# Performance work log

Measured on AMD Instinct MI355X. Metric: run time of the kernel, lower is better.

Reference implementation:

```python
import jax, jax.numpy as jnp
import numpy as np

MARGIN = 0.0  # init kwarg margin=0


def setup_inputs() -> dict:
    key = jax.random.key(0)
    k1, k2 = jax.random.split(key)
    inputs = jax.random.normal(k1, (4096, 2048), dtype=jnp.float32)
    targets = jax.random.randint(k2, (4096,), 0, 64, dtype=jnp.int64)
    return {"inputs": inputs, "targets": targets}


def _last_true_index(cond):
    # cond: (n, n) bool. Original torch loop zeros leading True entries until one
    # remains -> keeps the LAST True index per row.
    n = cond.shape[1]
    return (n - 1) - jnp.argmax(cond[:, ::-1], axis=1)


def reference(inputs, targets):
    n = inputs.shape[0]
    INF = jnp.asarray(jnp.inf, dtype=inputs.dtype)

    # pairwise euclidean distances: ||xi||^2 + ||xj||^2 - 2 xi.xj, clamp, sqrt
    sq = jnp.sum(inputs * inputs, axis=1)
    dist = sq[:, None] + sq[None, :] - 2.0 * (inputs @ inputs.T)
    dist = jnp.sqrt(jnp.clip(dist, 1e-12))  # (n, n)

    same = targets[:, None] == targets[None, :]  # (n, n) same-label mask

    # hardest positive / hardest negative per row
    dist_ap = jnp.where(same, dist, -INF).max(axis=1)
    dist_an = jnp.where(same, INF, dist).min(axis=1)

    # tie-broken indices (last occurrence, matching the torch loop)
    p = _last_true_index((dist == dist_ap[:, None]) & same)      # hardest pos idx
    q = _last_true_index((dist == dist_an[:, None]) & (~same))   # hardest neg idx

    # an2 = dist(hardest_pos_i, hardest_neg_i)
    dist_an2 = dist[p, q]

    # maskc: labels differing from both anchor's label and hardest-negative's label
    lbl_q = targets[q]
    maskc = (targets[None, :] != targets[:, None]) & (targets[None, :] != lbl_q[:, None])

    dist_q = dist[q]  # (n, n): distance rows of the hardest negatives
    ok_min = jnp.where(maskc, dist_q, INF).min(axis=1)
    r = _last_true_index((dist_q == ok_min[:, None]) & maskc)

    dist_an3 = dist[jnp.arange(n), r]  # dist(anchor, third-class sample)
    dist_an4 = dist_q[jnp.arange(n), r]  # dist(hardest neg, third-class sample) == ok_min

    # MarginRankingLoss(margin, reduce=False) with y=1: relu(ap - an + margin)
    loss = jax.nn.relu(dist_ap - dist_an + MARGIN)
    loss3 = jnp.abs(dist_an - dist_an2)
    loss4 = jnp.abs(dist_an3 - dist_an4)
    return (loss + loss3 + loss4).sum() / n
```

## Files before the change

kernel.cpp:

```cpp
#include <hip/hip_runtime.h>
#include <hip/hip_bf16.h>
#include <cstdint>

#define N_DIM 4096
#define K_DIM 2048
#define NKT 32
#define QSCALE 24.0f
#define QINV (1.0f / 24.0f)

typedef float floatx4 __attribute__((ext_vector_type(4)));
typedef int intx4 __attribute__((ext_vector_type(4)));
typedef unsigned short ushort8 __attribute__((ext_vector_type(8)));
typedef unsigned long long ull;

__device__ __forceinline__ unsigned short f2bf(float f) {
    unsigned int u = __builtin_bit_cast(unsigned int, f);
    unsigned int r = (u + 0x7fffu + ((u >> 16) & 1u)) >> 16;
    return (unsigned short)r;
}

__device__ __forceinline__ float bf2f(unsigned short b) {
    return __uint_as_float(((unsigned)b) << 16);
}

__device__ __forceinline__ void gld_lds16(const void* g, void* l) {
    __builtin_amdgcn_global_load_lds(
        (const __attribute__((address_space(1))) unsigned int*)g,
        (__attribute__((address_space(3))) unsigned int*)l,
        16, 0, 0);
}

__global__ __launch_bounds__(256)
void prep_kernel(const float* __restrict__ X, const int* __restrict__ tgt,
                 char* __restrict__ Qt, int* __restrict__ sqi,
                 char* __restrict__ tgt8) {
    const int row = blockIdx.x;
    const int tid = threadIdx.x;
    if (row < 16) tgt8[row * 256 + tid] = (char)tgt[row * 256 + tid];
    const float* xr = X + (size_t)row * K_DIM;
    floatx4 a = *(const floatx4*)(xr + tid * 8);
    floatx4 b = *(const floatx4*)(xr + tid * 8 + 4);
    int s = 0;
    unsigned lo = 0, hi = 0;
#pragma unroll
    for (int e = 0; e < 4; ++e) {
        int v = __float2int_rn(a[e] * QSCALE);
        v = min(127, max(-127, v));
        s += v * v;
        lo |= ((unsigned)(v & 0xff)) << (8 * e);
        int w = __float2int_rn(b[e] * QSCALE);
        w = min(127, max(-127, w));
        s += w * w;
        hi |= ((unsigned)(w & 0xff)) << (8 * e);
    }
    *(int2*)(Qt + ((size_t)(tid >> 1) * 4096 + row) * 16 + (tid & 1) * 8) =
        make_int2((int)lo, (int)hi);
#pragma unroll
    for (int off = 32; off; off >>= 1) s += __shfl_down(s, off);
    __shared__ int wsum[4];
    const int wave = tid >> 6, lane = tid & 63;
    if (lane == 0) wsum[wave] = s;
    __syncthreads();
    if (tid == 0) sqi[row] = wsum[0] + wsum[1] + wsum[2] + wsum[3];
}

#define BAR() __builtin_amdgcn_s_barrier()
#define PRIO1() __builtin_amdgcn_s_setprio(1)
#define PRIO0() __builtin_amdgcn_s_setprio(0)
#define VMCNT4() asm volatile("s_waitcnt vmcnt(4)" ::: "memory")
#define VMCNT0() asm volatile("s_waitcnt vmcnt(0)" ::: "memory")
#define MM8(MHI, AF) { _Pragma("unroll") for (int n_ = 0; n_ < 4; ++n_) { \
    _Pragma("unroll") for (int m_ = 0; m_ < 4; ++m_) { \
        acc[MHI][n_][m_] = __builtin_amdgcn_mfma_i32_16x16x64_i8( \
            AF[m_], bfv[n_], acc[MHI][n_][m_], 0, 0, 0); } } }
#define KTB 262144
#define STG_ALL(KT, BB) { \
    gld_lds16(bSt + (size_t)(KT) * KTB,        lds + (BB) + 16384 + widB); \
    gld_lds16(bSt + (size_t)(KT) * KTB + 2048, lds + (BB) + 24576 + widB); \
    gld_lds16(aSt + (size_t)(KT) * KTB,        lds + (BB) + widB); \
    gld_lds16(aSt + (size_t)(KT) * KTB + 2048, lds + (BB) + 8192 + widB); }

__global__ __launch_bounds__(512, 2)
void gemm_dist(const char* __restrict__ Qt, const int* __restrict__ sqi,
               unsigned short* __restrict__ Db) {
    __shared__ char lds[131072];
    const int tid = threadIdx.x;
    const int wid = tid >> 6, lane = tid & 63;
    const int wr = wid >> 2, wc = wid & 3;
    const int fr = lane & 15, ksub = lane >> 4;
    const int widB = wid * 1024;

    int rA[4], rB[4];
#pragma unroll
    for (int m = 0; m < 4; ++m) rA[m] = (ksub * 128 + m * 16 + fr) * 16;
#pragma unroll
    for (int n = 0; n < 4; ++n) rB[n] = (ksub * 128 + (wc & 1) * 64 + n * 16 + fr) * 16;
    const int aRegOff = wr * 8192;
    const int bRegOff = 16384 + (wc >> 1) * 8192;

    const int swz = (blockIdx.x & 7) * 32 + (blockIdx.x >> 3);
    const int bi = swz >> 4, bj = swz & 15;
    const int rowC0 = bi * 256, colC0 = bj * 256;

    const int srow = tid & 127;
    const int sks = tid >> 7;
    const char* aSt = Qt + ((size_t)sks * 4096 + rowC0 + srow) * 16;
    const char* bSt = Qt + ((size_t)sks * 4096 + colC0 + srow) * 16;

    intx4 acc[2][4][4];
#pragma unroll
    for (int a0 = 0; a0 < 2; ++a0)
#pragma unroll
    for (int a1 = 0; a1 < 4; ++a1)
#pragma unroll
    for (int a2 = 0; a2 < 4; ++a2) acc[a0][a1][a2] = (intx4){0, 0, 0, 0};
    intx4 aflo[4], afhi[4], bfv[4];

    STG_ALL(0, 0);
    STG_ALL(1, 32768);
    VMCNT4();
    BAR();

    int cb = 0, sb = 65536;
    for (int t = 0; t < NKT; ++t) {
        const char* bufA = lds + cb + aRegOff;
        const char* bufBp = lds + cb + bRegOff;
#pragma unroll
        for (int m = 0; m < 4; ++m) aflo[m] = *(const intx4*)(bufA + rA[m]);
#pragma unroll
        for (int m = 0; m < 4; ++m) afhi[m] = *(const intx4*)(bufA + 1024 + rA[m]);
#pragma unroll
        for (int n = 0; n < 4; ++n) bfv[n] = *(const intx4*)(bufBp + rB[n]);
        if (t < NKT - 2) { STG_ALL(t + 2, sb); VMCNT4(); }
        else if (t == NKT - 2) { VMCNT0(); }
        BAR();
        PRIO1(); MM8(0, aflo); MM8(1, afhi); PRIO0();
        cb += 32768; if (cb >= 131072) cb = 0;
        sb += 32768; if (sb >= 131072) sb = 0;
    }

#pragma unroll
    for (int MH = 0; MH < 2; ++MH)
#pragma unroll
    for (int n = 0; n < 4; ++n) {
        const int col = colC0 + wc * 64 + n * 16 + fr;
        const int sqc = sqi[col];
#pragma unroll
        for (int m = 0; m < 4; ++m) {
            const int row0 = rowC0 + wr * 128 + MH * 64 + m * 16 + ksub * 4;
#pragma unroll
            for (int r = 0; r < 4; ++r) {
                const int v = sqi[row0 + r] + sqc - 2 * acc[MH][n][m][r];
                const float d = (v > 0) ? sqrtf((float)v) * QINV : 1e-6f;
                Db[(size_t)(row0 + r) * N_DIM + col] = f2bf(d);
            }
        }
    }
}

__global__ __launch_bounds__(256)
void stats_loss(const unsigned short* __restrict__ Db, const char* __restrict__ tgt8,
                float* __restrict__ lossArr) {
    const int i = blockIdx.x, tid = threadIdx.x;
    const int lane = tid & 63, wave = tid >> 6;
    const int ti = tgt8[i];
    const unsigned short* row = Db + (size_t)i * N_DIM;
    ull kmax = 0ULL, kmin = ~0ULL;
#pragma unroll
    for (int it = 0; it < 2; ++it) {
        const int j0 = (it * 256 + tid) * 8;
        ushort8 d = *(const ushort8*)(row + j0);
        const ull tl8 = *(const ull*)(tgt8 + j0);
#pragma unroll
        for (int e = 0; e < 8; ++e) {
            const int j = j0 + e;
            const int tl = (int)((tl8 >> (8 * e)) & 0xff);
            const ull db = (ull)d[e] << 32;
            if (tl == ti) { ull k = db | (unsigned)j;  if (k > kmax) kmax = k; }
            else          { ull k = db | (unsigned)~j; if (k < kmin) kmin = k; }
        }
    }
#pragma unroll
    for (int off = 32; off; off >>= 1) {
        ull o = __shfl_xor(kmax, off); if (o > kmax) kmax = o;
        o = __shfl_xor(kmin, off);     if (o < kmin) kmin = o;
    }
    __shared__ ull sW[8];
    if (lane == 0) { sW[wave] = kmax; sW[4 + wave] = kmin; }
    __syncthreads();
    ull km = sW[0], kn = sW[4];
#pragma unroll
    for (int w2 = 1; w2 < 4; ++w2) {
        if (sW[w2] > km) km = sW[w2];
        if (sW[4 + w2] < kn) kn = sW[4 + w2];
    }
    const float ap = bf2f((unsigned short)(km >> 32));
    const int p = (int)(unsigned)(km & 0xFFFFFFFFu);
    const float an = bf2f((unsigned short)(kn >> 32));
    const int q = (int)~(unsigned)(kn & 0xFFFFFFFFu);

    const int lq = tgt8[q];
    const unsigned short* rowq = Db + (size_t)q * N_DIM;
    ull kr = ~0ULL;
#pragma unroll
    for (int it = 0; it < 2; ++it) {
        const int j0 = (it * 256 + tid) * 8;
        ushort8 d = *(const ushort8*)(rowq + j0);
        const ull tl8 = *(const ull*)(tgt8 + j0);
#pragma unroll
        for (int e = 0; e < 8; ++e) {
            const int j = j0 + e;
            const int tl = (int)((tl8 >> (8 * e)) & 0xff);
            if (tl != ti && tl != lq) {
                ull k = ((ull)d[e] << 32) | (unsigned)~j;
                if (k < kr) kr = k;
            }
        }
    }
#pragma unroll
    for (int off = 32; off; off >>= 1) {
        ull o = __shfl_xor(kr, off); if (o < kr) kr = o;
    }
    __shared__ ull sR[4];
    if (lane == 0) sR[wave] = kr;
    __syncthreads();
    if (tid == 0) {
        ull kk = sR[0];
#pragma unroll
        for (int w2 = 1; w2 < 4; ++w2) if (sR[w2] < kk) kk = sR[w2];
        const float okmin = bf2f((unsigned short)(kk >> 32));
        const int r = (int)~(unsigned)(kk & 0xFFFFFFFFu);
        const float an2 = bf2f(Db[(size_t)p * N_DIM + q]);
        const float an3 = bf2f(Db[(size_t)i * N_DIM + r]);
        lossArr[i] = fmaxf(ap - an, 0.f) + fabsf(an - an2) + fabsf(an3 - okmin);
    }
}

__global__ __launch_bounds__(256)
void finred(const float* __restrict__ lossArr, float* __restrict__ out) {
    const int tid = threadIdx.x;
    float s = 0.f;
    for (int j = tid; j < N_DIM; j += 256) s += lossArr[j];
#pragma unroll
    for (int off = 32; off; off >>= 1) s += __shfl_down(s, off);
    __shared__ float w[4];
    const int wave = tid >> 6, lane = tid & 63;
    if (lane == 0) w[wave] = s;
    __syncthreads();
    if (tid == 0) out[0] = (w[0] + w[1] + w[2] + w[3]) * (1.0f / (float)N_DIM);
}

extern "C" void kernel_launch(void* const* d_in, const int* in_sizes, int n_in,
                              void* d_out, int out_size, void* d_ws, size_t ws_size,
                              hipStream_t stream) {
    const float* X = (const float*)d_in[0];
    const int* tgt = (const int*)d_in[1];
    float* out = (float*)d_out;

    char* w = (char*)d_ws;
    char* Qt = w;
    unsigned short* Db = (unsigned short*)(w + ((size_t)16 << 20));
    int* sqi = (int*)(w + ((size_t)80 << 20));
    char* tgt8 = (char*)(sqi + N_DIM);
    float* lossArr = (float*)(tgt8 + 4096);

    prep_kernel<<<N_DIM, 256, 0, stream>>>(X, tgt, Qt, sqi, tgt8);
    gemm_dist<<<256, 512, 0, stream>>>(Qt, sqi, Db);
    stats_loss<<<N_DIM, 256, 0, stream>>>(Db, tgt8, lossArr);
    finred<<<1, 256, 0, stream>>>(lossArr, out);
}
```

Baseline: 76.79 us.

## Restructure int8 quantize prep to process 16 rows per block with LDS transpose

The prep kernel now handles 16 rows per block instead of one, looping over 16 K-chunks and staging the quantized int8 values in a double-buffered shared-memory tile. It then writes them to the transposed Qt layout as contiguous 256-byte runs per k-slice, replacing scattered 8-byte stores. The row sum-of-squares reduction becomes a 16-lane shuffle. This trades a one-row-per-block launch for fewer blocks and a barrier per chunk, which may reduce parallelism in the quantize step.

```diff
diff --git a/kernel.cpp b/kernel.cpp
--- a/kernel.cpp
+++ b/kernel.cpp
@@ -34,34 +34,42 @@
 void prep_kernel(const float* __restrict__ X, const int* __restrict__ tgt,
                  char* __restrict__ Qt, int* __restrict__ sqi,
                  char* __restrict__ tgt8) {
-    const int row = blockIdx.x;
+    __shared__ char sQ[4096];
     const int tid = threadIdx.x;
-    if (row < 16) tgt8[row * 256 + tid] = (char)tgt[row * 256 + tid];
-    const float* xr = X + (size_t)row * K_DIM;
-    floatx4 a = *(const floatx4*)(xr + tid * 8);
-    floatx4 b = *(const floatx4*)(xr + tid * 8 + 4);
+    const int rowC0 = blockIdx.x * 16;
+    if (blockIdx.x < 16) tgt8[blockIdx.x * 256 + tid] = (char)tgt[blockIdx.x * 256 + tid];
+    const int g = tid >> 4, l = tid & 15;
+    const float* xr = X + (size_t)(rowC0 + g) * K_DIM + l * 8;
+    const int wOff = (l >> 1) * 256 + g * 16 + (l & 1) * 8;
+    const int fksl = tid >> 5;
+    const int fr = (tid & 31) >> 1;
+    const int fh = tid & 1;
     int s = 0;
-    unsigned lo = 0, hi = 0;
-#pragma unroll
-    for (int e = 0; e < 4; ++e) {
-        int v = __float2int_rn(a[e] * QSCALE);
-        v = min(127, max(-127, v));
-        s += v * v;
-        lo |= ((unsigned)(v & 0xff)) << (8 * e);
-        int w = __float2int_rn(b[e] * QSCALE);
-        w = min(127, max(-127, w));
-        s += w * w;
-        hi |= ((unsigned)(w & 0xff)) << (8 * e);
-    }
-    *(int2*)(Qt + ((size_t)(tid >> 1) * 4096 + row) * 16 + (tid & 1) * 8) =
-        make_int2((int)lo, (int)hi);
-#pragma unroll
-    for (int off = 32; off; off >>= 1) s += __shfl_down(s, off);
-    __shared__ int wsum[4];
-    const int wave = tid >> 6, lane = tid & 63;
-    if (lane == 0) wsum[wave] = s;
-    __syncthreads();
-    if (tid == 0) sqi[row] = wsum[0] + wsum[1] + wsum[2] + wsum[3];
+    for (int ck = 0; ck < 16; ++ck) {
+        const int buf = (ck & 1) * 2048;
+        floatx4 a = *(const floatx4*)(xr + ck * 128);
+        floatx4 b = *(const floatx4*)(xr + ck * 128 + 4);
+        unsigned lo = 0, hi = 0;
+#pragma unroll
+        for (int e = 0; e < 4; ++e) {
+            int v = __float2int_rn(a[e] * QSCALE);
+            v = min(127, max(-127, v));
+            s += v * v;
+            lo |= ((unsigned)(v & 0xff)) << (8 * e);
+            int w2 = __float2int_rn(b[e] * QSCALE);
+            w2 = min(127, max(-127, w2));
+            s += w2 * w2;
+            hi |= ((unsigned)(w2 & 0xff)) << (8 * e);
+        }
+        *(int2*)(sQ + buf + wOff) = make_int2((int)lo, (int)hi);
+        __syncthreads();
+        const int2 val = *(const int2*)(sQ + buf + tid * 8);
+        const int ksg = ck * 8 + fksl;
+        *(int2*)(Qt + ((size_t)ksg * 4096 + rowC0 + fr) * 16 + fh * 8) = val;
+    }
+#pragma unroll
+    for (int off = 8; off; off >>= 1) s += __shfl_down(s, off, 16);
+    if (l == 0) sqi[rowC0 + g] = s;
 }
 
 #define BAR() __builtin_amdgcn_s_barrier()
@@ -264,7 +272,7 @@
     char* tgt8 = (char*)(sqi + N_DIM);
     float* lossArr = (float*)(tgt8 + 4096);
 
-    prep_kernel<<<N_DIM, 256, 0, stream>>>(X, tgt, Qt, sqi, tgt8);
+    prep_kernel<<<256, 256, 0, stream>>>(X, tgt, Qt, sqi, tgt8);
     gemm_dist<<<256, 512, 0, stream>>>(Qt, sqi, Db);
     stats_loss<<<N_DIM, 256, 0, stream>>>(Db, tgt8, lossArr);
     finred<<<1, 256, 0, stream>>>(lossArr, out);
```

Result: no change. 77.06 us (+0.4%).
